# Kernel optimization log

Hardware: AMD Instinct MI355X
Metric: run time of the kernel (lower is better)

## Reference

```python
import jax, jax.numpy as jnp
import numpy as np

TEMPERATURE = 0.07


def setup_inputs() -> dict:
    key = jax.random.key(0)
    k1, k2 = jax.random.split(key)
    B, D = 4096, 512
    emb1 = jax.random.normal(k1, (B, D), dtype=jnp.float32)
    emb2 = jax.random.normal(k2, (B, D), dtype=jnp.float32)
    # module assumes L2-normalised embeddings
    emb1 = emb1 / jnp.linalg.norm(emb1, axis=-1, keepdims=True)
    emb2 = emb2 / jnp.linalg.norm(emb2, axis=-1, keepdims=True)
    return {"emb1": emb1, "emb2": emb2}


def reference(emb1, emb2):
    B = emb1.shape[0]
    emb = jnp.concatenate([emb1, emb2], axis=0)            # (2B, D)
    sim = jnp.einsum('id,jd->ij', emb, emb) / TEMPERATURE  # (2B, 2B)
    neg_inf = jnp.finfo(sim.dtype).min
    self_mask = jnp.eye(2 * B, dtype=bool)
    sim = jnp.where(self_mask, neg_inf, sim)
    labels = jnp.concatenate([jnp.arange(B, 2 * B), jnp.arange(B)])
    logp = jax.nn.log_softmax(sim, axis=-1)                # stable softmax CE
    nll = -jnp.take_along_axis(logp, labels[:, None], axis=-1)[:, 0]
    return jnp.mean(nll)
```

## Files before the change

kernel.cpp:

```cpp
#include <hip/hip_runtime.h>
#include <hip/hip_bf16.h>

#define B_    4096
#define D_    512
#define TB_   8192
#define BM    128
#define BK    128
#define NK    4
#define NTILE 64
#define NTRI  2080
#define INV_T 14.285714285714286f
#define SCL   (INV_T / 16129.0f)

typedef __attribute__((ext_vector_type(4))) int   v4i;

#define GLOAD_LDS16(gp, lp)                                                        \
  __builtin_amdgcn_global_load_lds((const __attribute__((address_space(1))) void*)(gp), \
                                   (__attribute__((address_space(3))) void*)(lp),  \
                                   16, 0, 0)

__global__ void ntx_prep(const float* __restrict__ a, const float* __restrict__ b,
                         char* __restrict__ E8, float* __restrict__ L) {
  int t = blockIdx.x * blockDim.x + threadIdx.x;
  int i = t * 16;
  const float* src = (i < B_ * D_) ? (a + i) : (b + (i - B_ * D_));
  v4i o;
#pragma unroll
  for (int g = 0; g < 4; ++g) {
    float4 v = ((const float4*)src)[g];
    int q0 = __float2int_rn(v.x * 127.0f) & 255;
    int q1 = __float2int_rn(v.y * 127.0f) & 255;
    int q2 = __float2int_rn(v.z * 127.0f) & 255;
    int q3 = __float2int_rn(v.w * 127.0f) & 255;
    o[g] = q0 | (q1 << 8) | (q2 << 16) | (q3 << 24);
  }
  ((v4i*)E8)[t] = o;
  if (t < TB_) L[t] = 0.0f;
}

__global__ __launch_bounds__(256, 2)
void ntx_sim(const char* __restrict__ E8, float* __restrict__ L,
             float* __restrict__ pos) {
  __shared__ __align__(16) char As[BM * BK];
  __shared__ __align__(16) char Bs[BM * BK];

  const int bid = blockIdx.x;
  const int t   = (bid & 7) * (NTRI / 8) + (bid >> 3);
  int ti = (int)((129.0f - sqrtf(16641.0f - 8.0f * (float)t)) * 0.5f);
  while (ti * (129 - ti) / 2 > t) --ti;
  while ((ti + 1) * (128 - ti) / 2 <= t) ++ti;
  const int tj = ti + (t - ti * (129 - ti) / 2);
  const int rowTile = ti * BM, colTile = tj * BM;
  const bool diag = (ti == tj);
  const bool posT = (tj == ti + B_ / BM);

  const int tid = threadIdx.x, lane = tid & 63, wave = tid >> 6;
  const int wr = wave >> 1, wc = wave & 1;
  const int llo = lane & 15, lhi = lane >> 4;

  unsigned offA[4], offB[4], ldsOf[4];
#pragma unroll
  for (int r = 0; r < 4; ++r) {
    int ch = r * 256 + tid, row = ch >> 3;
    int sc = ((ch & 7) ^ (row & 7)) << 4;
    offA[r]  = (unsigned)(rowTile + row) * D_ + sc;
    offB[r]  = (unsigned)(colTile + row) * D_ + sc;
    ldsOf[r] = (unsigned)ch * 16;
  }
  unsigned fA[2][4], fB[2][4];
#pragma unroll
  for (int ks = 0; ks < 2; ++ks)
#pragma unroll
    for (int m = 0; m < 4; ++m) {
      int chc = ks * 4 + lhi;
      int ra  = wr * 64 + m * 16 + llo;
      fA[ks][m] = (unsigned)(ra * BK + (((unsigned)chc ^ (ra & 7)) << 4));
      int rb  = wc * 64 + m * 16 + llo;
      fB[ks][m] = (unsigned)(rb * BK + (((unsigned)chc ^ (rb & 7)) << 4));
    }

  v4i acc[4][4] = {};

  for (int kt = 0; kt < NK; ++kt) {
    const unsigned kb = (unsigned)kt * BK;
#pragma unroll
    for (int r = 0; r < 4; ++r) GLOAD_LDS16(E8 + offA[r] + kb, &As[ldsOf[r]]);
#pragma unroll
    for (int r = 0; r < 4; ++r) GLOAD_LDS16(E8 + offB[r] + kb, &Bs[ldsOf[r]]);
    __syncthreads();
#pragma unroll
    for (int ks = 0; ks < 2; ++ks) {
      v4i af[4], bf[4];
#pragma unroll
      for (int m = 0; m < 4; ++m) {
        af[m] = *(const v4i*)&As[fA[ks][m]];
        bf[m] = *(const v4i*)&Bs[fB[ks][m]];
      }
#pragma unroll
      for (int m = 0; m < 4; ++m)
#pragma unroll
        for (int n = 0; n < 4; ++n)
          acc[m][n] = __builtin_amdgcn_mfma_i32_16x16x64_i8(af[m], bf[n],
                                                            acc[m][n], 0, 0, 0);
    }
    __syncthreads();
  }

  float cs[4] = {0.f, 0.f, 0.f, 0.f};
#pragma unroll
  for (int m = 0; m < 4; ++m) {
    float rs[4] = {0.f, 0.f, 0.f, 0.f};
#pragma unroll
    for (int n = 0; n < 4; ++n) {
      int gc = colTile + wc * 64 + n * 16 + llo;
#pragma unroll
      for (int jj = 0; jj < 4; ++jj) {
        int gr = rowTile + wr * 64 + m * 16 + lhi * 4 + jj;
        float s = (float)acc[m][n][jj] * SCL;
        if (posT && gc - gr == B_) pos[gr] = s;
        float e = __expf(s);
        e = (diag && gr == gc) ? 0.0f : e;
        rs[jj] += e;
        cs[n]  += e;
      }
    }
#pragma unroll
    for (int jj = 0; jj < 4; ++jj) {
      float v = rs[jj];
      v += __shfl_xor(v, 1);
      v += __shfl_xor(v, 2);
      v += __shfl_xor(v, 4);
      v += __shfl_xor(v, 8);
      if (llo == 0) {
        int gr = rowTile + wr * 64 + m * 16 + lhi * 4 + jj;
        atomicAdd(&L[gr], v);
      }
    }
  }
  if (!diag) {
#pragma unroll
    for (int n = 0; n < 4; ++n) {
      float v = cs[n];
      v += __shfl_xor(v, 16);
      v += __shfl_xor(v, 32);
      if (lhi == 0) {
        int gc = colTile + wc * 64 + n * 16 + llo;
        atomicAdd(&L[gc], v);
      }
    }
  }
}

__global__ void ntx_fin(const float* __restrict__ L, const float* __restrict__ pos,
                        float* __restrict__ out) {
  int tid = threadIdx.x;
  float s = 0.f;
#pragma unroll
  for (int k = 0; k < TB_ / 256; ++k) {
    int r = k * 256 + tid;
    s += __logf(L[r]) - pos[r & (B_ - 1)];
  }
#pragma unroll
  for (int off = 1; off < 64; off <<= 1) s += __shfl_xor(s, off);
  __shared__ float sm[4];
  if ((tid & 63) == 0) sm[tid >> 6] = s;
  __syncthreads();
  if (tid == 0) out[0] = (sm[0] + sm[1] + sm[2] + sm[3]) * (1.0f / TB_);
}

extern "C" void kernel_launch(void* const* d_in, const int* in_sizes, int n_in,
                              void* d_out, int out_size, void* d_ws, size_t ws_size,
                              hipStream_t stream) {
  const float* e1 = (const float*)d_in[0];
  const float* e2 = (const float*)d_in[1];
  float* out = (float*)d_out;
  char* E8   = (char*)d_ws;
  float* L   = (float*)((char*)d_ws + (size_t)TB_ * D_);
  float* pos = L + TB_;

  ntx_prep<<<1024, 256, 0, stream>>>(e1, e2, E8, L);
  ntx_sim<<<NTRI, 256, 0, stream>>>(E8, L, pos);
  ntx_fin<<<1, 256, 0, stream>>>(L, pos, out);
}
```

Measured before the change: 62.00 us.

## Replace atomic row-sum accumulation with per-tile partial buffers and two-stage reduction

The similarity kernel now writes each tile's row and column exp-sums into a dedicated partial-sum slot, where before it atomically added them into a shared per-row array. This removes the zero-init of that array from the prep kernel and the contention of many atomics on the same addresses. The final step becomes a 32-block kernel that sums 128 partials per row, takes the log and reduces, followed by a tiny single-block kernel for the mean. The cost is an extra launch and roughly 4 MB of partial-sum traffic written and read back.

```diff
diff --git a/kernel.cpp b/kernel.cpp
--- a/kernel.cpp
+++ b/kernel.cpp
@@ -12,7 +12,7 @@
 #define INV_T 14.285714285714286f
 #define SCL   (INV_T / 16129.0f)
 
-typedef __attribute__((ext_vector_type(4))) int   v4i;
+typedef __attribute__((ext_vector_type(4))) int v4i;
 
 #define GLOAD_LDS16(gp, lp)                                                        \
   __builtin_amdgcn_global_load_lds((const __attribute__((address_space(1))) void*)(gp), \
@@ -20,7 +20,7 @@
                                    16, 0, 0)
 
 __global__ void ntx_prep(const float* __restrict__ a, const float* __restrict__ b,
-                         char* __restrict__ E8, float* __restrict__ L) {
+                         char* __restrict__ E8) {
   int t = blockIdx.x * blockDim.x + threadIdx.x;
   int i = t * 16;
   const float* src = (i < B_ * D_) ? (a + i) : (b + (i - B_ * D_));
@@ -35,11 +35,10 @@
     o[g] = q0 | (q1 << 8) | (q2 << 16) | (q3 << 24);
   }
   ((v4i*)E8)[t] = o;
-  if (t < TB_) L[t] = 0.0f;
 }
 
 __global__ __launch_bounds__(256, 2)
-void ntx_sim(const char* __restrict__ E8, float* __restrict__ L,
+void ntx_sim(const char* __restrict__ E8, float* __restrict__ P,
              float* __restrict__ pos) {
   __shared__ __align__(16) char As[BM * BK];
   __shared__ __align__(16) char Bs[BM * BK];
@@ -106,6 +105,8 @@
     __syncthreads();
   }
 
+  float* __restrict__ Prow = P + ((size_t)ti * 2 * NTILE + (size_t)tj * 2 + wc) * BM;
+  float* __restrict__ Pcol = P + ((size_t)tj * 2 * NTILE + (size_t)ti * 2 + wr) * BM;
   float cs[4] = {0.f, 0.f, 0.f, 0.f};
 #pragma unroll
   for (int m = 0; m < 4; ++m) {
@@ -131,41 +132,46 @@
       v += __shfl_xor(v, 2);
       v += __shfl_xor(v, 4);
       v += __shfl_xor(v, 8);
-      if (llo == 0) {
-        int gr = rowTile + wr * 64 + m * 16 + lhi * 4 + jj;
-        atomicAdd(&L[gr], v);
-      }
+      if (llo == 0) Prow[wr * 64 + m * 16 + lhi * 4 + jj] = v;
     }
   }
-  if (!diag) {
+  if (diag) {
+    ;
+  } else {
 #pragma unroll
     for (int n = 0; n < 4; ++n) {
       float v = cs[n];
       v += __shfl_xor(v, 16);
       v += __shfl_xor(v, 32);
-      if (lhi == 0) {
-        int gc = colTile + wc * 64 + n * 16 + llo;
-        atomicAdd(&L[gc], v);
-      }
+      if (lhi == 0) Pcol[wc * 64 + n * 16 + llo] = v;
     }
   }
 }
 
-__global__ void ntx_fin(const float* __restrict__ L, const float* __restrict__ pos,
-                        float* __restrict__ out) {
-  int tid = threadIdx.x;
+__global__ void ntx_fin1(const float* __restrict__ P, const float* __restrict__ pos,
+                         float* __restrict__ par) {
+  int r = blockIdx.x * 256 + threadIdx.x;
+  int ti = r >> 7, rloc = r & 127;
+  const float* base = P + (size_t)ti * 2 * NTILE * BM + rloc;
   float s = 0.f;
+#pragma unroll 16
+  for (int j = 0; j < 2 * NTILE; ++j) s += base[j * BM];
+  float nll = __logf(s) - pos[r & (B_ - 1)];
+  float v = nll;
 #pragma unroll
-  for (int k = 0; k < TB_ / 256; ++k) {
-    int r = k * 256 + tid;
-    s += __logf(L[r]) - pos[r & (B_ - 1)];
-  }
+  for (int off = 1; off < 64; off <<= 1) v += __shfl_xor(v, off);
+  __shared__ float sm[4];
+  if ((threadIdx.x & 63) == 0) sm[threadIdx.x >> 6] = v;
+  __syncthreads();
+  if (threadIdx.x == 0) par[blockIdx.x] = sm[0] + sm[1] + sm[2] + sm[3];
+}
+
+__global__ void ntx_fin2(const float* __restrict__ par, float* __restrict__ out) {
+  int t = threadIdx.x;
+  float s = (t < 32) ? par[t] : 0.f;
 #pragma unroll
-  for (int off = 1; off < 64; off <<= 1) s += __shfl_xor(s, off);
-  __shared__ float sm[4];
-  if ((tid & 63) == 0) sm[tid >> 6] = s;
-  __syncthreads();
-  if (tid == 0) out[0] = (sm[0] + sm[1] + sm[2] + sm[3]) * (1.0f / TB_);
+  for (int off = 1; off < 32; off <<= 1) s += __shfl_xor(s, off);
+  if (t == 0) out[0] = s * (1.0f / TB_);
 }
 
 extern "C" void kernel_launch(void* const* d_in, const int* in_sizes, int n_in,
@@ -174,11 +180,13 @@
   const float* e1 = (const float*)d_in[0];
   const float* e2 = (const float*)d_in[1];
   float* out = (float*)d_out;
-  char* E8   = (char*)d_ws;
-  float* L   = (float*)((char*)d_ws + (size_t)TB_ * D_);
-  float* pos = L + TB_;
+  char*  E8  = (char*)d_ws;
+  float* P   = (float*)((char*)d_ws + (size_t)TB_ * D_);
+  float* pos = P + (size_t)NTILE * 2 * NTILE * BM;
+  float* par = pos + B_;
 
-  ntx_prep<<<1024, 256, 0, stream>>>(e1, e2, E8, L);
-  ntx_sim<<<NTRI, 256, 0, stream>>>(E8, L, pos);
-  ntx_fin<<<1, 256, 0, stream>>>(L, pos, out);
+  ntx_prep<<<1024, 256, 0, stream>>>(e1, e2, E8);
+  ntx_sim<<<NTRI, 256, 0, stream>>>(E8, P, pos);
+  ntx_fin1<<<TB_ / 256, 256, 0, stream>>>(P, pos, par);
+  ntx_fin2<<<1, 64, 0, stream>>>(par, out);
 }
```

New measurement: 50.27 us. 18.9% less time.
